# Kernel tuning notes

Hardware: AMD Instinct MI355X
Metric: run time of the kernel (lower is better)

The kernel has to match this reference:

```python
import jax, jax.numpy as jnp
import numpy as np

N, E, D, IN_DIM, NUM_CLASSES, G, L = 50000, 800000, 128, 128, 10, 64, 3
BN_EPS = 1e-5


def _bn(h, gamma, beta, mean, var):
    # inference-mode batchnorm with running stats
    return (h - mean) * jax.lax.rsqrt(var + BN_EPS) * gamma + beta


def setup_inputs() -> dict:
    key = jax.random.key(0)
    ks = jax.random.split(key, 24)
    s = 0.02
    x = jax.random.normal(ks[0], (N, IN_DIM), dtype=jnp.float32)
    c_2 = jax.random.randint(ks[1], (E,), 0, N)
    u_2 = jax.random.randint(ks[2], (E,), 0, N)
    batch = jnp.sort(jax.random.randint(ks[3], (N,), 0, G))
    inp = {
        "x": x, "c_2": c_2, "u_2": u_2, "batch": batch,
        "We": jax.random.normal(ks[4], (IN_DIM, D)) * s,
        "be": jnp.zeros((D,), jnp.float32),
        # per-layer GIN MLP: Linear(d,2d) -> BN(2d) -> ReLU -> Linear(2d,d)
        "W1": jax.random.normal(ks[5], (L, D, 2 * D)) * s,
        "b1": jnp.zeros((L, 2 * D), jnp.float32),
        "g1": jnp.ones((L, 2 * D), jnp.float32),
        "bt1": jnp.zeros((L, 2 * D), jnp.float32),
        "m1": jax.random.normal(ks[6], (L, 2 * D)) * 0.1,
        "v1": jax.random.uniform(ks[7], (L, 2 * D), minval=0.5, maxval=1.5),
        "W2": jax.random.normal(ks[8], (L, 2 * D, D)) * s,
        "b2": jnp.zeros((L, D), jnp.float32),
        # post-conv BatchNorm(d)
        "g2": jnp.ones((L, D), jnp.float32),
        "bt2": jnp.zeros((L, D), jnp.float32),
        "m2": jax.random.normal(ks[9], (L, D)) * 0.1,
        "v2": jax.random.uniform(ks[10], (L, D), minval=0.5, maxval=1.5),
        # readout: Linear(d,d) -> ReLU -> (dropout off) -> Linear(d,num_classes)
        "Wr1": jax.random.normal(ks[11], (D, D)) * s,
        "br1": jnp.zeros((D,), jnp.float32),
        "Wr2": jax.random.normal(ks[12], (D, NUM_CLASSES)) * s,
        "br2": jnp.zeros((NUM_CLASSES,), jnp.float32),
    }
    return inp


def reference(x, c_2, u_2, batch, We, be, W1, b1, g1, bt1, m1, v1,
              W2, b2, g2, bt2, m2, v2, Wr1, br1, Wr2, br2):
    h = x @ We + be  # [N, D]
    for l in range(L):
        # GINConv (eps=0): h_i <- MLP(h_i + sum_{j->i} h_j)
        agg = jax.ops.segment_sum(h[c_2], u_2, num_segments=N)  # [N, D]
        z = h + agg
        z = jax.nn.relu(_bn(z @ W1[l] + b1[l], g1[l], bt1[l], m1[l], v1[l]))
        z = z @ W2[l] + b2[l]
        h = jax.nn.relu(_bn(z, g2[l], bt2[l], m2[l], v2[l]))
        # dropout: identity in eval mode
    pooled = jax.ops.segment_sum(h, batch, num_segments=G)  # [G, D]
    out = jax.nn.relu(pooled @ Wr1 + br1) @ Wr2 + br2  # [G, num_classes]
    return out
```

## Files before the change

### kernel.cpp

```cpp
#include <hip/hip_runtime.h>

#define BN_EPS 1e-5f

typedef __attribute__((ext_vector_type(8))) short bf16x8;
typedef __attribute__((ext_vector_type(4))) float f32x4;
typedef unsigned int uint32;

__device__ __forceinline__ unsigned short f2bf(float f) {
    unsigned u = __float_as_uint(f);
    u += 0x7FFFu + ((u >> 16) & 1u);
    return (unsigned short)(u >> 16);
}
__device__ __forceinline__ float bf2f(unsigned short u) {
    return __uint_as_float((unsigned)u << 16);
}
__device__ __forceinline__ float lo_bf(uint32 u) { return __uint_as_float(u << 16); }
__device__ __forceinline__ float hi_bf(uint32 u) { return __uint_as_float(u & 0xFFFF0000u); }
__device__ __forceinline__ uint32 pack_bf(float a0, float a1) {
    return ((uint32)f2bf(a1) << 16) | (uint32)f2bf(a0);
}

__global__ void init_kernel(int* __restrict__ deg, float* __restrict__ pooled, int N, int GP) {
    int i = blockIdx.x * 256 + threadIdx.x;
    if (i < N) deg[i] = 0;
    if (i < GP) pooled[i] = 0.f;
}

__global__ void count_deg_kernel(const int* __restrict__ u, int* __restrict__ deg, int E) {
    for (int e = blockIdx.x * blockDim.x + threadIdx.x; e < E; e += gridDim.x * blockDim.x)
        atomicAdd(&deg[u[e]], 1);
}

__global__ __launch_bounds__(256) void scan_local_kernel(const int* __restrict__ cnt,
                                                         int* __restrict__ start,
                                                         int* __restrict__ partials, int n) {
    __shared__ int buf[256];
    int i = blockIdx.x * 256 + threadIdx.x;
    int v = (i < n) ? cnt[i] : 0;
    buf[threadIdx.x] = v;
    __syncthreads();
    for (int off = 1; off < 256; off <<= 1) {
        int t = (threadIdx.x >= off) ? buf[threadIdx.x - off] : 0;
        __syncthreads();
        buf[threadIdx.x] += t;
        __syncthreads();
    }
    if (i < n) start[i] = buf[threadIdx.x] - v;
    if (threadIdx.x == 255) partials[blockIdx.x] = buf[255];
}

__global__ __launch_bounds__(256) void scan_add_kernel(int* __restrict__ node_start,
                                                       int* __restrict__ coarse_cursor,
                                                       const int* __restrict__ partials,
                                                       int nb, int n, int total) {
    __shared__ int buf[256];
    const int t = threadIdx.x;
    buf[t] = (t < nb) ? partials[t] : 0;
    __syncthreads();
    for (int off = 1; off < 256; off <<= 1) {
        int v = (t >= off) ? buf[t - off] : 0;
        __syncthreads();
        buf[t] += v;
        __syncthreads();
    }
    const int offset = (blockIdx.x == 0) ? 0 : buf[blockIdx.x - 1];
    int i = blockIdx.x * 256 + t;
    if (i < n) {
        int v = node_start[i] + offset;
        node_start[i] = v;
        if ((i & 255) == 0) coarse_cursor[i >> 8] = v;
    } else if (i == n) {
        node_start[n] = total;
    }
}

__global__ __launch_bounds__(256) void bin_coarse_kernel(const int* __restrict__ u2,
                                                         const int* __restrict__ c2,
                                                         int* __restrict__ coarse_cursor,
                                                         int* __restrict__ buck, int E) {
    __shared__ int lcnt[256];
    __shared__ int lbase[256];
    const int tid = threadIdx.x;
    lcnt[tid] = 0;
    __syncthreads();
    const int e0 = blockIdx.x * 4096;
    int ue[16];
#pragma unroll
    for (int k = 0; k < 16; ++k) {
        int e = e0 + k * 256 + tid;
        int u = (e < E) ? u2[e] : -1;
        ue[k] = u;
        if (u >= 0) atomicAdd(&lcnt[u >> 8], 1);
    }
    __syncthreads();
    int c0 = lcnt[tid];
    lbase[tid] = c0 ? atomicAdd(&coarse_cursor[tid], c0) : 0;
    lcnt[tid] = 0;
    __syncthreads();
#pragma unroll
    for (int k = 0; k < 16; ++k) {
        int e = e0 + k * 256 + tid;
        if (e < E) {
            int u = ue[k];
            int cb = u >> 8;
            int pos = lbase[cb] + atomicAdd(&lcnt[cb], 1);
            buck[pos] = ((u & 255) << 16) | c2[e];
        }
    }
}

__global__ __launch_bounds__(256) void bin_node_kernel(const int* __restrict__ node_start,
                                                       const int* __restrict__ buck,
                                                       int* __restrict__ csr_src, int N, int E) {
    __shared__ int lcur[256];
    const int cb = blockIdx.x;
    const int tid = threadIdx.x;
    int idx = cb * 256 + tid;
    lcur[tid] = (idx < N) ? node_start[idx] : E;
    __syncthreads();
    const int s = node_start[cb * 256];
    const int t_end = node_start[min(cb * 256 + 256, N)];
    for (int e = s + tid; e < t_end; e += 256) {
        int v = buck[e];
        int pos = atomicAdd(&lcur[v >> 16], 1);
        csr_src[pos] = v & 0xFFFF;
    }
}

__global__ __launch_bounds__(256) void aggregate_kernel(const unsigned short* __restrict__ h,
                                                        const int* __restrict__ row_start,
                                                        const int* __restrict__ csr_src,
                                                        unsigned short* __restrict__ h2, int N) {
    int node = blockIdx.x * 4 + (threadIdx.x >> 6);
    int lane = threadIdx.x & 63;
    if (node >= N) return;
    const int q = lane >> 4, sl = lane & 15;

    float a0 = 0.f, a1 = 0.f, a2 = 0.f, a3 = 0.f, a4 = 0.f, a5 = 0.f, a6 = 0.f, a7 = 0.f;
    if (q == 0) {
        uint4 v = ((const uint4*)(h + (size_t)node * 128))[sl];
        a0 = lo_bf(v.x); a1 = hi_bf(v.x); a2 = lo_bf(v.y); a3 = hi_bf(v.y);
        a4 = lo_bf(v.z); a5 = hi_bf(v.z); a6 = lo_bf(v.w); a7 = hi_bf(v.w);
    }

    const int rs = row_start[node], re = row_start[node + 1];
    int e = rs;
    for (; e + 16 <= re; e += 16) {
        int s0 = csr_src[e + q];
        int s1 = csr_src[e + 4 + q];
        int s2 = csr_src[e + 8 + q];
        int s3 = csr_src[e + 12 + q];
        uint4 v0 = ((const uint4*)(h + (size_t)s0 * 128))[sl];
        uint4 v1 = ((const uint4*)(h + (size_t)s1 * 128))[sl];
        uint4 v2 = ((const uint4*)(h + (size_t)s2 * 128))[sl];
        uint4 v3 = ((const uint4*)(h + (size_t)s3 * 128))[sl];
        a0 += (lo_bf(v0.x) + lo_bf(v1.x)) + (lo_bf(v2.x) + lo_bf(v3.x));
        a1 += (hi_bf(v0.x) + hi_bf(v1.x)) + (hi_bf(v2.x) + hi_bf(v3.x));
        a2 += (lo_bf(v0.y) + lo_bf(v1.y)) + (lo_bf(v2.y) + lo_bf(v3.y));
        a3 += (hi_bf(v0.y) + hi_bf(v1.y)) + (hi_bf(v2.y) + hi_bf(v3.y));
        a4 += (lo_bf(v0.z) + lo_bf(v1.z)) + (lo_bf(v2.z) + lo_bf(v3.z));
        a5 += (hi_bf(v0.z) + hi_bf(v1.z)) + (hi_bf(v2.z) + hi_bf(v3.z));
        a6 += (lo_bf(v0.w) + lo_bf(v1.w)) + (lo_bf(v2.w) + lo_bf(v3.w));
        a7 += (hi_bf(v0.w) + hi_bf(v1.w)) + (hi_bf(v2.w) + hi_bf(v3.w));
    }
    for (; e + 8 <= re; e += 8) {
        int s0 = csr_src[e + q];
        int s1 = csr_src[e + 4 + q];
        uint4 v = ((const uint4*)(h + (size_t)s0 * 128))[sl];
        uint4 w = ((const uint4*)(h + (size_t)s1 * 128))[sl];
        a0 += lo_bf(v.x) + lo_bf(w.x); a1 += hi_bf(v.x) + hi_bf(w.x);
        a2 += lo_bf(v.y) + lo_bf(w.y); a3 += hi_bf(v.y) + hi_bf(w.y);
        a4 += lo_bf(v.z) + lo_bf(w.z); a5 += hi_bf(v.z) + hi_bf(w.z);
        a6 += lo_bf(v.w) + lo_bf(w.w); a7 += hi_bf(v.w) + hi_bf(w.w);
    }
    for (; e + 4 <= re; e += 4) {
        int s0 = csr_src[e + q];
        uint4 v = ((const uint4*)(h + (size_t)s0 * 128))[sl];
        a0 += lo_bf(v.x); a1 += hi_bf(v.x); a2 += lo_bf(v.y); a3 += hi_bf(v.y);
        a4 += lo_bf(v.z); a5 += hi_bf(v.z); a6 += lo_bf(v.w); a7 += hi_bf(v.w);
    }
    if (q < re - e) {
        int s0 = csr_src[e + q];
        uint4 v = ((const uint4*)(h + (size_t)s0 * 128))[sl];
        a0 += lo_bf(v.x); a1 += hi_bf(v.x); a2 += lo_bf(v.y); a3 += hi_bf(v.y);
        a4 += lo_bf(v.z); a5 += hi_bf(v.z); a6 += lo_bf(v.w); a7 += hi_bf(v.w);
    }

    a0 += __shfl_xor(a0, 16, 64); a0 += __shfl_xor(a0, 32, 64);
    a1 += __shfl_xor(a1, 16, 64); a1 += __shfl_xor(a1, 32, 64);
    a2 += __shfl_xor(a2, 16, 64); a2 += __shfl_xor(a2, 32, 64);
    a3 += __shfl_xor(a3, 16, 64); a3 += __shfl_xor(a3, 32, 64);
    a4 += __shfl_xor(a4, 16, 64); a4 += __shfl_xor(a4, 32, 64);
    a5 += __shfl_xor(a5, 16, 64); a5 += __shfl_xor(a5, 32, 64);
    a6 += __shfl_xor(a6, 16, 64); a6 += __shfl_xor(a6, 32, 64);
    a7 += __shfl_xor(a7, 16, 64); a7 += __shfl_xor(a7, 32, 64);

    if (q == 0) {
        uint4 o;
        o.x = pack_bf(a0, a1); o.y = pack_bf(a2, a3);
        o.z = pack_bf(a4, a5); o.w = pack_bf(a6, a7);
        ((uint4*)(h2 + (size_t)node * 128))[sl] = o;
    }
}

__global__ void prep_kernel(const float* __restrict__ We, const float* __restrict__ W1,
                            const float* __restrict__ W2,
                            unsigned short* __restrict__ Wte,
                            unsigned short* __restrict__ Wt1,
                            unsigned short* __restrict__ Wt2,
                            const float* __restrict__ be,
                            const float* __restrict__ b1, const float* __restrict__ g1,
                            const float* __restrict__ bt1, const float* __restrict__ m1,
                            const float* __restrict__ v1,
                            const float* __restrict__ b2, const float* __restrict__ g2,
                            const float* __restrict__ bt2, const float* __restrict__ m2,
                            const float* __restrict__ v2,
                            float* __restrict__ sce, float* __restrict__ she,
                            float* __restrict__ sc1, float* __restrict__ sh1,
                            float* __restrict__ sc2, float* __restrict__ sh2, int L) {
    int y = blockIdx.y;
    int t = threadIdx.x;
    if (blockIdx.x == 0) {
        if (y == 0) {
            if (t < 128) { sce[t] = 1.f; she[t] = be[t]; }
        } else if (y <= L) {
            int o = (y - 1) * 256 + t;
            float s = g1[o] * rsqrtf(v1[o] + BN_EPS);
            sc1[o] = s;
            sh1[o] = (b1[o] - m1[o]) * s + bt1[o];
        } else {
            if (t < 128) {
                int o = (y - L - 1) * 128 + t;
                float s = g2[o] * rsqrtf(v2[o] + BN_EPS);
                sc2[o] = s;
                sh2[o] = (b2[o] - m2[o]) * s + bt2[o];
            }
        }
    }
    const float* src;
    unsigned short* dst;
    int K;
    if (y == 0)      { src = We; dst = Wte; K = 128; }
    else if (y <= L) { int l = y - 1;     src = W1 + (size_t)l * 128 * 256; dst = Wt1 + (size_t)l * 128 * 256; K = 128; }
    else             { int l = y - L - 1; src = W2 + (size_t)l * 256 * 128; dst = Wt2 + (size_t)l * 256 * 128; K = 256; }
    int idx = blockIdx.x * 256 + t;
    int OUT = 32768 / K;
    if (y == 0) { if (idx >= 128 * 128) return; OUT = 128; }
    int c = idx / K, k = idx % K;
    dst[idx] = f2bf(src[(size_t)k * OUT + c]);
}

template <int K, int OUT, bool RELU, bool A_F32>
__global__ __launch_bounds__(256) void mfma_gemm_kernel(
    const void* __restrict__ Ap, const unsigned short* __restrict__ Wt,
    const float* __restrict__ scale, const float* __restrict__ shift,
    unsigned short* __restrict__ Cout, int nrows)
{
    constexpr int NT = OUT / 16;
    constexpr int KS = K / 32;
    constexpr int CH = OUT * K / 8;
    __shared__ unsigned short WtLds[OUT * K];

    const int tid = threadIdx.x;
    {
        const float4* src = (const float4*)Wt;
#pragma unroll
        for (int i = 0; i < CH / 256; ++i) {
            int c = tid + i * 256;
            int row = c / (K / 8);
            unsigned off = ((unsigned)c * 16u) ^ (((unsigned)row & 7u) << 4);
            *(float4*)((char*)WtLds + off) = src[c];
        }
    }
    __syncthreads();

    const int lane = tid & 63;
    const int l15 = lane & 15, lhi = lane >> 4;
    const int rbase = blockIdx.x * 128 + (tid >> 6) * 32;
    const int r0 = rbase + l15;
    const int r1 = rbase + 16 + l15;
    const int rr0 = min(r0, nrows - 1);
    const int rr1 = min(r1, nrows - 1);

    bf16x8 bfrag[2][KS];
    if constexpr (A_F32) {
        const float* a0 = (const float*)Ap + (size_t)rr0 * K + lhi * 8;
        const float* a1 = (const float*)Ap + (size_t)rr1 * K + lhi * 8;
#pragma unroll
        for (int ks = 0; ks < KS; ++ks) {
            float4 u0 = *(const float4*)(a0 + ks * 32);
            float4 u1 = *(const float4*)(a0 + ks * 32 + 4);
            float4 w0 = *(const float4*)(a1 + ks * 32);
            float4 w1 = *(const float4*)(a1 + ks * 32 + 4);
            bf16x8 f, g;
            f[0] = (short)f2bf(u0.x); f[1] = (short)f2bf(u0.y);
            f[2] = (short)f2bf(u0.z); f[3] = (short)f2bf(u0.w);
            f[4] = (short)f2bf(u1.x); f[5] = (short)f2bf(u1.y);
            f[6] = (short)f2bf(u1.z); f[7] = (short)f2bf(u1.w);
            g[0] = (short)f2bf(w0.x); g[1] = (short)f2bf(w0.y);
            g[2] = (short)f2bf(w0.z); g[3] = (short)f2bf(w0.w);
            g[4] = (short)f2bf(w1.x); g[5] = (short)f2bf(w1.y);
            g[6] = (short)f2bf(w1.z); g[7] = (short)f2bf(w1.w);
            bfrag[0][ks] = f;
            bfrag[1][ks] = g;
        }
    } else {
        const unsigned short* a0 = (const unsigned short*)Ap + (size_t)rr0 * K + lhi * 8;
        const unsigned short* a1 = (const unsigned short*)Ap + (size_t)rr1 * K + lhi * 8;
#pragma unroll
        for (int ks = 0; ks < KS; ++ks) {
            bfrag[0][ks] = *(const bf16x8*)(a0 + ks * 32);
            bfrag[1][ks] = *(const bf16x8*)(a1 + ks * 32);
        }
    }

    f32x4 acc[2][NT];
#pragma unroll
    for (int g = 0; g < 2; ++g)
#pragma unroll
        for (int nt = 0; nt < NT; ++nt) acc[g][nt] = (f32x4){0.f, 0.f, 0.f, 0.f};

#pragma unroll
    for (int ks = 0; ks < KS; ++ks) {
#pragma unroll
        for (int nt = 0; nt < NT; ++nt) {
            int row = nt * 16 + l15;
            unsigned off = ((unsigned)((row * K + ks * 32 + lhi * 8) * 2)) ^ (((unsigned)(l15 & 7u)) << 4);
            bf16x8 wfrag = *(const bf16x8*)((const char*)WtLds + off);
            acc[0][nt] = __builtin_amdgcn_mfma_f32_16x16x32_bf16(wfrag, bfrag[0][ks], acc[0][nt], 0, 0, 0);
            acc[1][nt] = __builtin_amdgcn_mfma_f32_16x16x32_bf16(wfrag, bfrag[1][ks], acc[1][nt], 0, 0, 0);
        }
    }

    const float4* sc4 = (const float4*)scale;
    const float4* sh4 = (const float4*)shift;
#pragma unroll
    for (int g = 0; g < 2; ++g) {
        const int r = (g == 0) ? r0 : r1;
        if (r >= nrows) continue;
#pragma unroll
        for (int nt = 0; nt < NT; ++nt) {
            float4 sc = sc4[nt * 4 + lhi];
            float4 sh = sh4[nt * 4 + lhi];
            float y0 = acc[g][nt][0] * sc.x + sh.x;
            float y1 = acc[g][nt][1] * sc.y + sh.y;
            float y2 = acc[g][nt][2] * sc.z + sh.z;
            float y3 = acc[g][nt][3] * sc.w + sh.w;
            if (RELU) {
                y0 = fmaxf(y0, 0.f); y1 = fmaxf(y1, 0.f);
                y2 = fmaxf(y2, 0.f); y3 = fmaxf(y3, 0.f);
            }
            size_t o = (size_t)r * OUT + nt * 16 + lhi * 4;
            ushort4 p = make_ushort4(f2bf(y0), f2bf(y1), f2bf(y2), f2bf(y3));
            *(ushort4*)(Cout + o) = p;
        }
    }
}

__global__ __launch_bounds__(128) void pool_kernel(const unsigned short* __restrict__ h,
                                                   const int* __restrict__ batch,
                                                   float* __restrict__ pooled, int N, int chunk) {
    int d = threadIdx.x;
    int start = blockIdx.x * chunk;
    if (start >= N) return;
    int end = min(start + chunk, N);
    float acc = 0.f;
    int g = batch[start];
    for (int r = start; r < end; ++r) {
        int bg = batch[r];
        if (bg != g) {
            atomicAdd(&pooled[g * 128 + d], acc);
            acc = 0.f;
            g = bg;
        }
        acc += bf2f(h[(size_t)r * 128 + d]);
    }
    atomicAdd(&pooled[g * 128 + d], acc);
}

__global__ __launch_bounds__(128) void readout_kernel(const float* __restrict__ pooled,
                                                      const float* __restrict__ Wr1,
                                                      const float* __restrict__ br1,
                                                      const float* __restrict__ Wr2,
                                                      const float* __restrict__ br2,
                                                      float* __restrict__ out) {
    __shared__ float prow[128];
    __shared__ float t[128];
    int g = blockIdx.x, j = threadIdx.x;
    prow[j] = pooled[g * 128 + j];
    __syncthreads();
    float acc = 0.f;
    for (int k = 0; k < 128; ++k) acc += prow[k] * Wr1[k * 128 + j];
    t[j] = fmaxf(acc + br1[j], 0.f);
    __syncthreads();
    if (j < 10) {
        float a2 = 0.f;
        for (int k = 0; k < 128; ++k) a2 += t[k] * Wr2[k * 10 + j];
        out[g * 10 + j] = a2 + br2[j];
    }
}

extern "C" void kernel_launch(void* const* d_in, const int* in_sizes, int n_in,
                              void* d_out, int out_size, void* d_ws, size_t ws_size,
                              hipStream_t stream) {
    const float* x   = (const float*)d_in[0];
    const int* c2    = (const int*)d_in[1];
    const int* u2    = (const int*)d_in[2];
    const int* batch = (const int*)d_in[3];
    const float* We  = (const float*)d_in[4];
    const float* be  = (const float*)d_in[5];
    const float* W1  = (const float*)d_in[6];
    const float* b1  = (const float*)d_in[7];
    const float* g1  = (const float*)d_in[8];
    const float* bt1 = (const float*)d_in[9];
    const float* m1  = (const float*)d_in[10];
    const float* v1  = (const float*)d_in[11];
    const float* W2  = (const float*)d_in[12];
    const float* b2  = (const float*)d_in[13];
    const float* g2  = (const float*)d_in[14];
    const float* bt2 = (const float*)d_in[15];
    const float* m2  = (const float*)d_in[16];
    const float* v2  = (const float*)d_in[17];
    const float* Wr1 = (const float*)d_in[18];
    const float* br1 = (const float*)d_in[19];
    const float* Wr2 = (const float*)d_in[20];
    const float* br2 = (const float*)d_in[21];

    const int N = in_sizes[3];
    const int E = in_sizes[1];
    const int L = in_sizes[7] / 256;
    const int G = out_size / 10;

    const int NC = (N + 255) / 256;

    char* ws = (char*)d_ws;
    size_t off = 0;
    auto alloc = [&](size_t bytes) { char* p = ws + off; off += (bytes + 255) & ~(size_t)255; return p; };
    unsigned short* hb   = (unsigned short*)alloc((size_t)N * 128 * 2);
    unsigned short* h2b  = (unsigned short*)alloc((size_t)N * 128 * 2);
    unsigned short* zb   = (unsigned short*)alloc((size_t)N * 256 * 2);
    unsigned short* Wte  = (unsigned short*)alloc(128 * 128 * 2);
    unsigned short* Wt1  = (unsigned short*)alloc((size_t)L * 256 * 128 * 2);
    unsigned short* Wt2  = (unsigned short*)alloc((size_t)L * 128 * 256 * 2);
    float* sce = (float*)alloc(128 * 4);
    float* she = (float*)alloc(128 * 4);
    float* sc1 = (float*)alloc((size_t)L * 256 * 4);
    float* sh1 = (float*)alloc((size_t)L * 256 * 4);
    float* sc2 = (float*)alloc((size_t)L * 128 * 4);
    float* sh2 = (float*)alloc((size_t)L * 128 * 4);
    float* pooled = (float*)alloc((size_t)G * 128 * 4);
    int* deg        = (int*)alloc((size_t)N * 4);
    int* node_start = (int*)alloc((size_t)(N + 1) * 4);
    int* coarse_cursor = (int*)alloc(256 * 4);
    int* partials   = (int*)alloc(256 * 4);
    int* buck       = (int*)alloc((size_t)E * 4);
    int* csr_src    = (int*)alloc((size_t)E * 4);

    init_kernel<<<(max(N, G * 128) + 255) / 256, 256, 0, stream>>>(deg, pooled, N, G * 128);
    count_deg_kernel<<<1024, 256, 0, stream>>>(u2, deg, E);
    const int scan_blocks = (N + 255) / 256;
    scan_local_kernel<<<scan_blocks, 256, 0, stream>>>(deg, node_start, partials, N);
    scan_add_kernel<<<(N + 256) / 256, 256, 0, stream>>>(node_start, coarse_cursor, partials,
                                                         scan_blocks, N, E);
    bin_coarse_kernel<<<(E + 4095) / 4096, 256, 0, stream>>>(u2, c2, coarse_cursor, buck, E);
    bin_node_kernel<<<NC, 256, 0, stream>>>(node_start, buck, csr_src, N, E);

    prep_kernel<<<dim3((256 * 128 + 255) / 256, 1 + 2 * L), 256, 0, stream>>>(
        We, W1, W2, Wte, Wt1, Wt2,
        be, b1, g1, bt1, m1, v1, b2, g2, bt2, m2, v2,
        sce, she, sc1, sh1, sc2, sh2, L);

    const int gemm_blocks = (N + 127) / 128;

    mfma_gemm_kernel<128, 128, false, true><<<gemm_blocks, 256, 0, stream>>>(
        x, Wte, sce, she, hb, N);

    for (int l = 0; l < L; ++l) {
        aggregate_kernel<<<(N + 3) / 4, 256, 0, stream>>>(hb, node_start, csr_src, h2b, N);
        mfma_gemm_kernel<128, 256, true, false><<<gemm_blocks, 256, 0, stream>>>(
            h2b, Wt1 + (size_t)l * 128 * 256, sc1 + l * 256, sh1 + l * 256, zb, N);
        mfma_gemm_kernel<256, 128, true, false><<<gemm_blocks, 256, 0, stream>>>(
            zb, Wt2 + (size_t)l * 256 * 128, sc2 + l * 128, sh2 + l * 128, hb, N);
    }

    const int chunk = (N + 511) / 512;
    pool_kernel<<<512, 128, 0, stream>>>(hb, batch, pooled, N, chunk);
    readout_kernel<<<G, 128, 0, stream>>>(pooled, Wr1, br1, Wr2, br2, (float*)d_out);
}
```

Baseline: 322.3 us.

## Build CSR via coarse-bucket counting and move weight swizzle into prep

Replaces the per-node degree count plus two-level global scan with a coarse count over 256-node buckets, a single-block scan, and per-bucket local counting and scanning inside bin_node_kernel, which now writes node_start itself. This removes the global per-node atomics, the N-sized scans and several launches, at the cost of an extra pass over the bucket entries in bin_node. Separately, the XOR bank swizzle of the transposed weights is now applied once in prep_kernel, so each GEMM block copies weights into LDS linearly instead of computing swizzled addresses.

```diff
diff --git a/kernel.cpp b/kernel.cpp
--- a/kernel.cpp
+++ b/kernel.cpp
@@ -20,58 +20,41 @@
     return ((uint32)f2bf(a1) << 16) | (uint32)f2bf(a0);
 }
 
-__global__ void init_kernel(int* __restrict__ deg, float* __restrict__ pooled, int N, int GP) {
-    int i = blockIdx.x * 256 + threadIdx.x;
-    if (i < N) deg[i] = 0;
-    if (i < GP) pooled[i] = 0.f;
-}
-
-__global__ void count_deg_kernel(const int* __restrict__ u, int* __restrict__ deg, int E) {
-    for (int e = blockIdx.x * blockDim.x + threadIdx.x; e < E; e += gridDim.x * blockDim.x)
-        atomicAdd(&deg[u[e]], 1);
-}
-
-__global__ __launch_bounds__(256) void scan_local_kernel(const int* __restrict__ cnt,
-                                                         int* __restrict__ start,
-                                                         int* __restrict__ partials, int n) {
-    __shared__ int buf[256];
-    int i = blockIdx.x * 256 + threadIdx.x;
-    int v = (i < n) ? cnt[i] : 0;
-    buf[threadIdx.x] = v;
-    __syncthreads();
-    for (int off = 1; off < 256; off <<= 1) {
-        int t = (threadIdx.x >= off) ? buf[threadIdx.x - off] : 0;
-        __syncthreads();
-        buf[threadIdx.x] += t;
-        __syncthreads();
-    }
-    if (i < n) start[i] = buf[threadIdx.x] - v;
-    if (threadIdx.x == 255) partials[blockIdx.x] = buf[255];
-}
-
-__global__ __launch_bounds__(256) void scan_add_kernel(int* __restrict__ node_start,
-                                                       int* __restrict__ coarse_cursor,
-                                                       const int* __restrict__ partials,
-                                                       int nb, int n, int total) {
+__global__ __launch_bounds__(256) void count_coarse_kernel(const int* __restrict__ u2,
+                                                           int* __restrict__ coarse_cnt, int E) {
+    __shared__ int lcnt[256];
+    const int tid = threadIdx.x;
+    lcnt[tid] = 0;
+    __syncthreads();
+    const int e0 = blockIdx.x * 4096;
+#pragma unroll
+    for (int k = 0; k < 16; ++k) {
+        int e = e0 + k * 256 + tid;
+        if (e < E) atomicAdd(&lcnt[u2[e] >> 8], 1);
+    }
+    __syncthreads();
+    int c = lcnt[tid];
+    if (c) atomicAdd(&coarse_cnt[tid], c);
+}
+
+__global__ __launch_bounds__(256) void scan_coarse_kernel(const int* __restrict__ coarse_cnt,
+                                                          int* __restrict__ coarse_start,
+                                                          int* __restrict__ coarse_cursor,
+                                                          int nc, int total) {
     __shared__ int buf[256];
     const int t = threadIdx.x;
-    buf[t] = (t < nb) ? partials[t] : 0;
+    int v = (t < nc) ? coarse_cnt[t] : 0;
+    buf[t] = v;
     __syncthreads();
     for (int off = 1; off < 256; off <<= 1) {
-        int v = (t >= off) ? buf[t - off] : 0;
+        int x = (t >= off) ? buf[t - off] : 0;
         __syncthreads();
-        buf[t] += v;
+        buf[t] += x;
         __syncthreads();
     }
-    const int offset = (blockIdx.x == 0) ? 0 : buf[blockIdx.x - 1];
-    int i = blockIdx.x * 256 + t;
-    if (i < n) {
-        int v = node_start[i] + offset;
-        node_start[i] = v;
-        if ((i & 255) == 0) coarse_cursor[i >> 8] = v;
-    } else if (i == n) {
-        node_start[n] = total;
-    }
+    int excl = buf[t] - v;
+    if (t <= nc) coarse_start[t] = (t < nc) ? excl : total;
+    if (t < nc) coarse_cursor[t] = excl;
 }
 
 __global__ __launch_bounds__(256) void bin_coarse_kernel(const int* __restrict__ u2,
@@ -109,21 +92,40 @@
     }
 }
 
-__global__ __launch_bounds__(256) void bin_node_kernel(const int* __restrict__ node_start,
+__global__ __launch_bounds__(256) void bin_node_kernel(const int* __restrict__ coarse_start,
                                                        const int* __restrict__ buck,
-                                                       int* __restrict__ csr_src, int N, int E) {
+                                                       int* __restrict__ node_start,
+                                                       int* __restrict__ csr_src, int N) {
+    __shared__ int lcnt[256];
     __shared__ int lcur[256];
     const int cb = blockIdx.x;
     const int tid = threadIdx.x;
+    const int s = coarse_start[cb];
+    const int t_end = coarse_start[cb + 1];
+    lcnt[tid] = 0;
+    __syncthreads();
+    for (int e = s + tid; e < t_end; e += 256)
+        atomicAdd(&lcnt[buck[e] >> 16], 1);
+    __syncthreads();
+    int v = lcnt[tid];
+    lcur[tid] = v;
+    __syncthreads();
+    for (int off = 1; off < 256; off <<= 1) {
+        int x = (tid >= off) ? lcur[tid - off] : 0;
+        __syncthreads();
+        lcur[tid] += x;
+        __syncthreads();
+    }
+    int excl = lcur[tid] - v;
+    int gstart = s + excl;
     int idx = cb * 256 + tid;
-    lcur[tid] = (idx < N) ? node_start[idx] : E;
-    __syncthreads();
-    const int s = node_start[cb * 256];
-    const int t_end = node_start[min(cb * 256 + 256, N)];
+    if (idx <= N) node_start[idx] = gstart;
+    lcur[tid] = gstart;
+    __syncthreads();
     for (int e = s + tid; e < t_end; e += 256) {
-        int v = buck[e];
-        int pos = atomicAdd(&lcur[v >> 16], 1);
-        csr_src[pos] = v & 0xFFFF;
+        int w = buck[e];
+        int pos = atomicAdd(&lcur[w >> 16], 1);
+        csr_src[pos] = w & 0xFFFF;
     }
 }
 
@@ -247,7 +249,8 @@
     int OUT = 32768 / K;
     if (y == 0) { if (idx >= 128 * 128) return; OUT = 128; }
     int c = idx / K, k = idx % K;
-    dst[idx] = f2bf(src[(size_t)k * OUT + c]);
+    unsigned byte = ((unsigned)(idx * 2)) ^ (((unsigned)c & 7u) << 4);
+    *(unsigned short*)((char*)dst + byte) = f2bf(src[(size_t)k * OUT + c]);
 }
 
 template <int K, int OUT, bool RELU, bool A_F32>
@@ -267,9 +270,7 @@
 #pragma unroll
         for (int i = 0; i < CH / 256; ++i) {
             int c = tid + i * 256;
-            int row = c / (K / 8);
-            unsigned off = ((unsigned)c * 16u) ^ (((unsigned)row & 7u) << 4);
-            *(float4*)((char*)WtLds + off) = src[c];
+            ((float4*)WtLds)[c] = src[c];
         }
     }
     __syncthreads();
@@ -449,21 +450,21 @@
     float* sc2 = (float*)alloc((size_t)L * 128 * 4);
     float* sh2 = (float*)alloc((size_t)L * 128 * 4);
     float* pooled = (float*)alloc((size_t)G * 128 * 4);
-    int* deg        = (int*)alloc((size_t)N * 4);
-    int* node_start = (int*)alloc((size_t)(N + 1) * 4);
+    int* coarse_cnt    = (int*)alloc(256 * 4);
+    int* coarse_start  = (int*)alloc(257 * 4);
     int* coarse_cursor = (int*)alloc(256 * 4);
-    int* partials   = (int*)alloc(256 * 4);
-    int* buck       = (int*)alloc((size_t)E * 4);
-    int* csr_src    = (int*)alloc((size_t)E * 4);
-
-    init_kernel<<<(max(N, G * 128) + 255) / 256, 256, 0, stream>>>(deg, pooled, N, G * 128);
-    count_deg_kernel<<<1024, 256, 0, stream>>>(u2, deg, E);
-    const int scan_blocks = (N + 255) / 256;
-    scan_local_kernel<<<scan_blocks, 256, 0, stream>>>(deg, node_start, partials, N);
-    scan_add_kernel<<<(N + 256) / 256, 256, 0, stream>>>(node_start, coarse_cursor, partials,
-                                                         scan_blocks, N, E);
-    bin_coarse_kernel<<<(E + 4095) / 4096, 256, 0, stream>>>(u2, c2, coarse_cursor, buck, E);
-    bin_node_kernel<<<NC, 256, 0, stream>>>(node_start, buck, csr_src, N, E);
+    int* node_start    = (int*)alloc((size_t)(N + 1) * 4);
+    int* buck          = (int*)alloc((size_t)E * 4);
+    int* csr_src       = (int*)alloc((size_t)E * 4);
+
+    const int ebins = (E + 4095) / 4096;
+
+    hipMemsetAsync(coarse_cnt, 0, 256 * 4, stream);
+    hipMemsetAsync(pooled, 0, (size_t)G * 128 * 4, stream);
+    count_coarse_kernel<<<ebins, 256, 0, stream>>>(u2, coarse_cnt, E);
+    scan_coarse_kernel<<<1, 256, 0, stream>>>(coarse_cnt, coarse_start, coarse_cursor, NC, E);
+    bin_coarse_kernel<<<ebins, 256, 0, stream>>>(u2, c2, coarse_cursor, buck, E);
+    bin_node_kernel<<<NC, 256, 0, stream>>>(coarse_start, buck, node_start, csr_src, N);
 
     prep_kernel<<<dim3((256 * 128 + 255) / 256, 1 + 2 * L), 256, 0, stream>>>(
         We, W1, W2, Wte, Wt1, Wt2,
```

After: 295.3 us. 8.4% less time.
